# Kernel tuning notes

Hardware: AMD Instinct MI355X
Metric: run time of the kernel (lower is better)

The kernel has to match this reference:

```python
import jax, jax.numpy as jnp
import numpy as np

HEAD_SIZE = 64
NEG_INF = float('-inf')


def setup_inputs() -> dict:
    key = jax.random.key(0)
    ks = jax.random.split(key, 4)
    B, S, H, D = 8, 4096, 1024, HEAD_SIZE
    scale = 1.0 / np.sqrt(H)
    return {
        'x': jax.random.normal(ks[0], (B, S, H), dtype=jnp.float32),
        'Wq': jax.random.normal(ks[1], (H, D), dtype=jnp.float32) * scale,
        'bq': jnp.zeros((D,), dtype=jnp.float32),
        'Wk': jax.random.normal(ks[2], (H, D), dtype=jnp.float32) * scale,
        'bk': jnp.zeros((D,), dtype=jnp.float32),
        'Wv': jax.random.normal(ks[3], (H, D), dtype=jnp.float32) * scale,
        'bv': jnp.zeros((D,), dtype=jnp.float32),
    }


def reference(x, Wq, bq, Wk, bk, Wv, bv):
    # x: [B, S, H]; projections -> [B, S, D]
    B, S, H = x.shape
    q = jnp.einsum('bsh,hd->bsd', x, Wq) + bq
    k = jnp.einsum('bsh,hd->bsd', x, Wk) + bk
    v = jnp.einsum('bsh,hd->bsd', x, Wv) + bv
    # raw scores [B, S, S]
    scores = jnp.einsum('bqd,bkd->bqk', q, k)
    # causal mask applied BEFORE scaling (matches original; -inf/scale == -inf)
    causal = jnp.tril(jnp.ones((S, S), dtype=bool))
    scores = jnp.where(causal, scores, NEG_INF)
    scale = 1.0 / jnp.sqrt(jnp.asarray(q.shape[-1], dtype=scores.dtype))
    attn = jax.nn.softmax(scores * scale, axis=-1)
    # dropout = 0.0 (eval) -> identity
    return jnp.einsum('bqk,bkd->bqd', attn, v)
```

## Files before the change

### kernel.cpp

```cpp
#include <hip/hip_runtime.h>
#include <hip/hip_bf16.h>
#include <math.h>

#define SEQ 4096
#define HID 1024
#define DH  64
#define NB  8
#define QSCALE 0.18033688011112042f

typedef unsigned short ushort_t;
typedef unsigned int   uint_t;
typedef __attribute__((ext_vector_type(8)))  short  bf16x8;
typedef __attribute__((ext_vector_type(4)))  float  f32x4;
typedef __attribute__((ext_vector_type(16))) float  f32x16;
typedef __attribute__((ext_vector_type(4)))  uint_t u32x4;
typedef __attribute__((ext_vector_type(2)))  uint_t u32x2;

static __device__ __forceinline__ ushort_t f2bf(float f) {
    __hip_bfloat16 h = __float2bfloat16(f);
    return *reinterpret_cast<ushort_t*>(&h);
}
static __device__ __forceinline__ ushort_t f2bf_fast(float f) {
    uint_t u = __float_as_uint(f);
    return (ushort_t)((u + 0x8000u) >> 16);
}
static __device__ __forceinline__ uint_t bfpair(float lo, float hi) {
    return (uint_t)f2bf_fast(lo) | ((uint_t)f2bf_fast(hi) << 16);
}

static __device__ __forceinline__ void gld_lds16(const void* g, void* s) {
    __builtin_amdgcn_global_load_lds(
        (const __attribute__((address_space(1))) void*)g,
        (__attribute__((address_space(3))) void*)s, 16, 0, 0);
}

__global__ __launch_bounds__(256) void prep_w(
    const float* __restrict__ Wq, const float* __restrict__ Wk,
    const float* __restrict__ Wv, ushort_t* __restrict__ wts)
{
    __shared__ ushort_t tr[64][72];
    const int bx   = blockIdx.x;
    const int mmat = bx >> 4;
    const int kt   = bx & 15;
    const float* W  = (mmat == 0) ? Wq : (mmat == 1) ? Wk : Wv;
    const float  sc = (mmat == 0) ? QSCALE : 1.0f;

    const int t  = threadIdx.x;
    const int kr = t >> 2, kc = (t & 3) * 16;
    const float* src = W + (size_t)(kt * 64 + kr) * DH + kc;
    float4 a0 = *(const float4*)(src);
    float4 a1 = *(const float4*)(src + 4);
    float4 a2 = *(const float4*)(src + 8);
    float4 a3 = *(const float4*)(src + 12);
    float vv[16] = {a0.x,a0.y,a0.z,a0.w, a1.x,a1.y,a1.z,a1.w,
                    a2.x,a2.y,a2.z,a2.w, a3.x,a3.y,a3.z,a3.w};
    #pragma unroll
    for (int i = 0; i < 16; ++i) tr[kr][kc + i] = f2bf(vv[i] * sc);
    __syncthreads();

    const int cl = t >> 2, jc = (t & 3) * 16;
    const int c  = mmat * 64 + cl;
    ushort_t* dst = wts + kt * 12288 + c * 64;
    #pragma unroll
    for (int jj = 0; jj < 16; ++jj) {
        int j = jc + jj;
        dst[((j >> 3) ^ (cl & 7)) * 8 + (j & 7)] = tr[j][cl];
    }
}

__global__ __launch_bounds__(256) void qkv_proj(
    const float* __restrict__ x, const ushort_t* __restrict__ wts,
    const float* __restrict__ bq, const float* __restrict__ bk,
    const float* __restrict__ bv,
    ushort_t* __restrict__ qimg, ushort_t* __restrict__ kimg,
    ushort_t* __restrict__ vimg)
{
    __shared__ ushort_t bw[2][12288];

    const int t  = threadIdx.x;
    const int w  = t >> 6, l = t & 63, lr = l & 15, g = l >> 4;
    const int row0 = blockIdx.x * 64;
    const int row  = row0 + w * 16 + lr;
    const int ch0 = (g ^ (lr & 7)) * 8;
    const int ch1 = ((g + 4) ^ (lr & 7)) * 8;

    f32x4 acc[12];
    #pragma unroll
    for (int i = 0; i < 12; ++i) acc[i] = (f32x4){0.f,0.f,0.f,0.f};

    const char* wbase = (const char*)wts;
    const int   wlo   = w * 1024 + l * 16;
    const float* xrow = x + (size_t)row * HID + g * 8;

    float4 Xa0, Xa1, Xb0, Xb1;
    {
        Xa0 = *(const float4*)(xrow);
        Xa1 = *(const float4*)(xrow + 4);
        Xb0 = *(const float4*)(xrow + 32);
        Xb1 = *(const float4*)(xrow + 36);
        char* bdst = (char*)&bw[0][0] + w * 1024;
        #pragma unroll
        for (int i = 0; i < 6; ++i)
            gld_lds16(wbase + wlo + i * 4096, bdst + i * 4096);
    }

    for (int kt = 0; kt < 16; ++kt) {
        const int buf = kt & 1;
        __syncthreads();
        float4 Na0, Na1, Nb0, Nb1;
        if (kt < 15) {
            const float* xn = xrow + (kt + 1) * 64;
            Na0 = *(const float4*)(xn);
            Na1 = *(const float4*)(xn + 4);
            Nb0 = *(const float4*)(xn + 32);
            Nb1 = *(const float4*)(xn + 36);
            char* bdst = (char*)&bw[buf ^ 1][0] + w * 1024;
            const char* bsrc = wbase + (size_t)(kt + 1) * 24576 + wlo;
            #pragma unroll
            for (int i = 0; i < 6; ++i)
                gld_lds16(bsrc + i * 4096, bdst + i * 4096);
        }
        bf16x8 af0, af1;
        {
            u32x4 p;
            p.x = bfpair(Xa0.x, Xa0.y); p.y = bfpair(Xa0.z, Xa0.w);
            p.z = bfpair(Xa1.x, Xa1.y); p.w = bfpair(Xa1.z, Xa1.w);
            af0 = *(bf16x8*)&p;
            u32x4 q;
            q.x = bfpair(Xb0.x, Xb0.y); q.y = bfpair(Xb0.z, Xb0.w);
            q.z = bfpair(Xb1.x, Xb1.y); q.w = bfpair(Xb1.z, Xb1.w);
            af1 = *(bf16x8*)&q;
        }
        #pragma unroll
        for (int ct = 0; ct < 12; ++ct) {
            const int c = ct * 16 + lr;
            bf16x8 b0 = *(bf16x8*)&bw[buf][c * 64 + ch0];
            bf16x8 b1 = *(bf16x8*)&bw[buf][c * 64 + ch1];
            acc[ct] = __builtin_amdgcn_mfma_f32_16x16x32_bf16(af0, b0, acc[ct], 0, 0, 0);
            acc[ct] = __builtin_amdgcn_mfma_f32_16x16x32_bf16(af1, b1, acc[ct], 0, 0, 0);
        }
        Xa0 = Na0; Xa1 = Na1; Xb0 = Nb0; Xb1 = Nb1;
    }

    #pragma unroll
    for (int ct = 0; ct < 12; ++ct) {
        const int c    = ct * 16 + lr;
        const int mmat = c >> 6;
        const int cc   = c & 63;
        const float* bp = (mmat == 0) ? bq : (mmat == 1) ? bk : bv;
        const float bias = bp[cc] * (mmat == 0 ? QSCALE : 1.0f);
        #pragma unroll
        for (int r = 0; r < 4; ++r) {
            const int s = row0 + w * 16 + g * 4 + r;
            const ushort_t v = f2bf_fast(acc[ct][r] + bias);
            if (mmat == 0)
                qimg[(size_t)s * 64 + cc] = v;
            else if (mmat == 1)
                kimg[(size_t)(s >> 6) * 4096 + (s & 63) * 64 +
                     ((cc >> 3) ^ (s & 7)) * 8 + (cc & 7)] = v;
            else
                vimg[(size_t)(s >> 6) * 4096 + (size_t)cc * 64 +
                     (((s & 63) >> 3) ^ (cc & 7)) * 8 + (s & 7)] = v;
        }
    }
}

__global__ __launch_bounds__(256) void attn(
    const ushort_t* __restrict__ qimg, const ushort_t* __restrict__ kimg,
    const ushort_t* __restrict__ vimg,
    float* __restrict__ Opart, float* __restrict__ Lpart)
{
    __shared__ ushort_t kvs[2][8192];
    __shared__ float    osc[4096];
    __shared__ float    lred[2][32];

    const int t  = threadIdx.x;
    const int w  = t >> 6, l = t & 63, lw = l & 31, hs = l >> 5;
    const int qh = w & 1;
    const int kh = w >> 1;
    const int bx   = blockIdx.x;
    const int half = bx & 1;
    const int u    = bx >> 1;
    const int qt   = 63 - (u >> 3);
    const int b    = u & 7;
    const int q0   = qt * 64;
    const int n    = qt + 1, hn = n >> 1;
    const int t0   = half ? hn : 0;
    const int t1   = half ? n : hn;
    const int qq   = q0 + qh * 32 + lw;

    bf16x8 qf[4];
    {
        const ushort_t* qp = qimg + (size_t)(b * SEQ + qq) * 64 + hs * 8;
        #pragma unroll
        for (int ks = 0; ks < 4; ++ks) qf[ks] = *(const bf16x8*)(qp + ks * 16);
    }

    f32x16 o0, o1;
    #pragma unroll
    for (int r = 0; r < 16; ++r) { o0[r] = 0.f; o1[r] = 0.f; }
    float lpart = 0.f;

    const char* kbase = (const char*)kimg + (size_t)b * 524288;
    const char* vbase = (const char*)vimg + (size_t)b * 524288;
    const int wo = w * 1024;
    const int lo = l * 16;

    if (t0 < t1) {
        const char* ks = kbase + (size_t)t0 * 8192;
        const char* vs = vbase + (size_t)t0 * 8192;
        char* lk = (char*)&kvs[0][0];
        gld_lds16(ks + wo + lo,        lk + wo);
        gld_lds16(ks + wo + lo + 4096, lk + wo + 4096);
        gld_lds16(vs + wo + lo,        lk + wo + 8192);
        gld_lds16(vs + wo + lo + 4096, lk + wo + 12288);
    }

    for (int kt = t0; kt < t1; ++kt) {
        const int cur = (kt - t0) & 1;
        __syncthreads();
        if (kt + 1 < t1) {
            const char* ks = kbase + (size_t)(kt + 1) * 8192;
            const char* vs = vbase + (size_t)(kt + 1) * 8192;
            char*       lk = (char*)&kvs[cur ^ 1][0];
            gld_lds16(ks + wo + lo,        lk + wo);
            gld_lds16(ks + wo + lo + 4096, lk + wo + 4096);
            gld_lds16(vs + wo + lo,        lk + wo + 8192);
            gld_lds16(vs + wo + lo + 4096, lk + wo + 12288);
        }

        const ushort_t* kb   = &kvs[cur][0];
        const int       krow = kh * 32 + lw;
        const ushort_t* krb  = kb + krow * 64;
        f32x16 s;
        #pragma unroll
        for (int r = 0; r < 16; ++r) s[r] = 0.f;
        #pragma unroll
        for (int ks = 0; ks < 4; ++ks) {
            bf16x8 kf = *(const bf16x8*)(krb + (((ks * 2 + hs) ^ (krow & 7)) * 8));
            s = __builtin_amdgcn_mfma_f32_32x32x16_bf16(kf, qf[ks], s, 0, 0, 0);
        }

        float p[16];
        if (kt == qt) {
            #pragma unroll
            for (int r = 0; r < 16; ++r) {
                const int kvg = kt * 64 + kh * 32 + (r & 3) + 8 * (r >> 2) + 4 * hs;
                p[r] = (kvg > qq) ? 0.f : __builtin_amdgcn_exp2f(s[r]);
            }
        } else {
            #pragma unroll
            for (int r = 0; r < 16; ++r) p[r] = __builtin_amdgcn_exp2f(s[r]);
        }
        {
            float s0 = (p[0] + p[1])  + (p[2] + p[3]);
            float s1 = (p[4] + p[5])  + (p[6] + p[7]);
            float s2 = (p[8] + p[9])  + (p[10] + p[11]);
            float s3 = (p[12] + p[13]) + (p[14] + p[15]);
            lpart += (s0 + s1) + (s2 + s3);
        }

        const ushort_t* vb = &kvs[cur][4096];
        #pragma unroll
        for (int ks2 = 0; ks2 < 2; ++ks2) {
            uint_t a0 = bfpair(p[ks2*8 + 0], p[ks2*8 + 1]);
            uint_t b0 = bfpair(p[ks2*8 + 4], p[ks2*8 + 5]);
            uint_t a1 = bfpair(p[ks2*8 + 2], p[ks2*8 + 3]);
            uint_t b1 = bfpair(p[ks2*8 + 6], p[ks2*8 + 7]);
            asm("v_permlane32_swap_b32 %0, %1" : "+v"(a0), "+v"(b0));
            asm("v_permlane32_swap_b32 %0, %1" : "+v"(a1), "+v"(b1));
            u32x4 pw = { a0, a1, b0, b1 };
            bf16x8 paf = *(bf16x8*)&pw;
            const int sl8 = kh * 4 + ks2 * 2 + hs;
            {
                const int vr0 = lw;
                bf16x8 vf0 = *(const bf16x8*)(vb + vr0 * 64 + ((sl8 ^ (vr0 & 7)) * 8));
                o0 = __builtin_amdgcn_mfma_f32_32x32x16_bf16(paf, vf0, o0, 0, 0, 0);
                const int vr1 = 32 + lw;
                bf16x8 vf1 = *(const bf16x8*)(vb + vr1 * 64 + ((sl8 ^ (vr1 & 7)) * 8));
                o1 = __builtin_amdgcn_mfma_f32_32x32x16_bf16(paf, vf1, o1, 0, 0, 0);
            }
        }
    }

    if (kh == 1) {
        const int lbase = (qh * 64 + l) * 32;
        #pragma unroll
        for (int i = 0; i < 4; ++i) {
            f32x4 v = { o0[4*i], o0[4*i+1], o0[4*i+2], o0[4*i+3] };
            *(f32x4*)&osc[lbase + ((i ^ (l & 7)) * 4)] = v;
        }
        #pragma unroll
        for (int i = 0; i < 4; ++i) {
            f32x4 v = { o1[4*i], o1[4*i+1], o1[4*i+2], o1[4*i+3] };
            *(f32x4*)&osc[lbase + (((i + 4) ^ (l & 7)) * 4)] = v;
        }
        float lsum = lpart + __shfl_xor(lpart, 32);
        if (hs == 0) lred[qh][lw] = lsum;
    }
    __syncthreads();
    if (kh == 0) {
        const int lbase = (qh * 64 + l) * 32;
        #pragma unroll
        for (int i = 0; i < 4; ++i) {
            f32x4 v = *(const f32x4*)&osc[lbase + ((i ^ (l & 7)) * 4)];
            o0[4*i] += v.x; o0[4*i+1] += v.y; o0[4*i+2] += v.z; o0[4*i+3] += v.w;
        }
        #pragma unroll
        for (int i = 0; i < 4; ++i) {
            f32x4 v = *(const f32x4*)&osc[lbase + (((i + 4) ^ (l & 7)) * 4)];
            o1[4*i] += v.x; o1[4*i+1] += v.y; o1[4*i+2] += v.z; o1[4*i+3] += v.w;
        }
        const float lt = (lpart + __shfl_xor(lpart, 32)) + lred[qh][lw];

        const int m = b * 64 + qt;
        float* Op = Opart + ((size_t)half * 512 + m) * 4096;
        #pragma unroll
        for (int r = 0; r < 16; ++r) {
            const int qrow = qh * 32 + (r & 3) + 8 * (r >> 2) + 4 * hs;
            Op[qrow * 64 + lw]      = o0[r];
            Op[qrow * 64 + 32 + lw] = o1[r];
        }
        if (hs == 0)
            Lpart[((size_t)half * 512 + m) * 64 + qh * 32 + lw] = lt;
    }
}

__global__ __launch_bounds__(256) void merge_o(
    const float* __restrict__ Opart, const float* __restrict__ Lpart,
    float* __restrict__ outg)
{
    const int m = blockIdx.x;
    const int b = m >> 6, qt = m & 63;
    const int t = threadIdx.x;
    const int row = t >> 2, c = (t & 3) * 16;

    const float* A = Opart + (size_t)m * 4096 + row * 64 + c;
    const float* B = Opart + (size_t)(512 + m) * 4096 + row * 64 + c;
    const float la = Lpart[(size_t)m * 64 + row];
    const float lb = Lpart[(size_t)(512 + m) * 64 + row];
    const float inv = 1.0f / (la + lb);
    float* dst = outg + ((size_t)b * SEQ + qt * 64 + row) * 64 + c;
    #pragma unroll
    for (int j = 0; j < 4; ++j) {
        float4 va = *(const float4*)(A + j * 4);
        float4 vb = *(const float4*)(B + j * 4);
        float4 vo = { (va.x + vb.x) * inv, (va.y + vb.y) * inv,
                      (va.z + vb.z) * inv, (va.w + vb.w) * inv };
        *(float4*)(dst + j * 4) = vo;
    }
}

extern "C" void kernel_launch(void* const* d_in, const int* in_sizes, int n_in,
                              void* d_out, int out_size, void* d_ws, size_t ws_size,
                              hipStream_t stream) {
    const float* x  = (const float*)d_in[0];
    const float* Wq = (const float*)d_in[1];
    const float* bq = (const float*)d_in[2];
    const float* Wk = (const float*)d_in[3];
    const float* bk = (const float*)d_in[4];
    const float* Wv = (const float*)d_in[5];
    const float* bv = (const float*)d_in[6];
    float* out = (float*)d_out;

    const size_t per = (size_t)NB * SEQ * DH;
    ushort_t* q   = (ushort_t*)d_ws;
    ushort_t* k   = q + per;
    ushort_t* v   = k + per;
    ushort_t* wts = v + per;
    float* Opart  = (float*)((char*)d_ws + (size_t)(16u << 20));
    float* Lpart  = (float*)((char*)d_ws + (size_t)(40u << 20));

    prep_w  <<<dim3(48),   256, 0, stream>>>(Wq, Wk, Wv, wts);
    qkv_proj<<<dim3(512),  256, 0, stream>>>(x, wts, bq, bk, bv, q, k, v);
    attn    <<<dim3(1024), 256, 0, stream>>>(q, k, v, Opart, Lpart);
    merge_o <<<dim3(512),  256, 0, stream>>>(Opart, Lpart, out);
}
```

Before: 257.1 us.

## Use persistent attention blocks with per-batch atomic work queues and XCD affinity

Switches the attention kernel from a fixed 1024-block grid to 768 persistent blocks. Each block pulls work items (query tile and half) from per-batch atomic counters, starting with the batch matching its XCD id so that K/V for one batch stays in that XCD's L2. Items are still issued longest-first. This aims to improve load balance across the triangular causal workload and L2 locality, at the cost of atomic traffic, extra barriers and a counter reset in prep_w.

```diff
diff --git a/kernel.cpp b/kernel.cpp
--- a/kernel.cpp
+++ b/kernel.cpp
@@ -36,8 +36,11 @@
 
 __global__ __launch_bounds__(256) void prep_w(
     const float* __restrict__ Wq, const float* __restrict__ Wk,
-    const float* __restrict__ Wv, ushort_t* __restrict__ wts)
+    const float* __restrict__ Wv, ushort_t* __restrict__ wts,
+    uint_t* __restrict__ cnt)
 {
+    if (blockIdx.x == 0 && threadIdx.x < 8) cnt[threadIdx.x] = 0;
+
     __shared__ ushort_t tr[64][72];
     const int bx   = blockIdx.x;
     const int mmat = bx >> 4;
@@ -168,161 +171,175 @@
 __global__ __launch_bounds__(256) void attn(
     const ushort_t* __restrict__ qimg, const ushort_t* __restrict__ kimg,
     const ushort_t* __restrict__ vimg,
-    float* __restrict__ Opart, float* __restrict__ Lpart)
+    float* __restrict__ Opart, float* __restrict__ Lpart,
+    uint_t* __restrict__ cnt)
 {
     __shared__ ushort_t kvs[2][8192];
     __shared__ float    osc[4096];
     __shared__ float    lred[2][32];
+    __shared__ int      jsh;
 
     const int t  = threadIdx.x;
     const int w  = t >> 6, l = t & 63, lw = l & 31, hs = l >> 5;
     const int qh = w & 1;
     const int kh = w >> 1;
-    const int bx   = blockIdx.x;
-    const int half = bx & 1;
-    const int u    = bx >> 1;
-    const int qt   = 63 - (u >> 3);
-    const int b    = u & 7;
-    const int q0   = qt * 64;
-    const int n    = qt + 1, hn = n >> 1;
-    const int t0   = half ? hn : 0;
-    const int t1   = half ? n : hn;
-    const int qq   = q0 + qh * 32 + lw;
-
-    bf16x8 qf[4];
-    {
-        const ushort_t* qp = qimg + (size_t)(b * SEQ + qq) * 64 + hs * 8;
-        #pragma unroll
-        for (int ks = 0; ks < 4; ++ks) qf[ks] = *(const bf16x8*)(qp + ks * 16);
-    }
-
-    f32x16 o0, o1;
-    #pragma unroll
-    for (int r = 0; r < 16; ++r) { o0[r] = 0.f; o1[r] = 0.f; }
-    float lpart = 0.f;
-
-    const char* kbase = (const char*)kimg + (size_t)b * 524288;
-    const char* vbase = (const char*)vimg + (size_t)b * 524288;
     const int wo = w * 1024;
     const int lo = l * 16;
 
-    if (t0 < t1) {
-        const char* ks = kbase + (size_t)t0 * 8192;
-        const char* vs = vbase + (size_t)t0 * 8192;
-        char* lk = (char*)&kvs[0][0];
-        gld_lds16(ks + wo + lo,        lk + wo);
-        gld_lds16(ks + wo + lo + 4096, lk + wo + 4096);
-        gld_lds16(vs + wo + lo,        lk + wo + 8192);
-        gld_lds16(vs + wo + lo + 4096, lk + wo + 12288);
-    }
-
-    for (int kt = t0; kt < t1; ++kt) {
-        const int cur = (kt - t0) & 1;
-        __syncthreads();
-        if (kt + 1 < t1) {
-            const char* ks = kbase + (size_t)(kt + 1) * 8192;
-            const char* vs = vbase + (size_t)(kt + 1) * 8192;
-            char*       lk = (char*)&kvs[cur ^ 1][0];
-            gld_lds16(ks + wo + lo,        lk + wo);
-            gld_lds16(ks + wo + lo + 4096, lk + wo + 4096);
-            gld_lds16(vs + wo + lo,        lk + wo + 8192);
-            gld_lds16(vs + wo + lo + 4096, lk + wo + 12288);
-        }
-
-        const ushort_t* kb   = &kvs[cur][0];
-        const int       krow = kh * 32 + lw;
-        const ushort_t* krb  = kb + krow * 64;
-        f32x16 s;
-        #pragma unroll
-        for (int r = 0; r < 16; ++r) s[r] = 0.f;
-        #pragma unroll
-        for (int ks = 0; ks < 4; ++ks) {
-            bf16x8 kf = *(const bf16x8*)(krb + (((ks * 2 + hs) ^ (krow & 7)) * 8));
-            s = __builtin_amdgcn_mfma_f32_32x32x16_bf16(kf, qf[ks], s, 0, 0, 0);
-        }
-
-        float p[16];
-        if (kt == qt) {
+    int xcd;
+    { int v; asm("s_getreg_b32 %0, hwreg(HW_REG_XCC_ID)" : "=s"(v)); xcd = v & 7; }
+
+    for (int pass = 0; pass < 8; ++pass) {
+        const int b = (xcd + pass) & 7;
+        const char* kbase = (const char*)kimg + (size_t)b * 524288;
+        const char* vbase = (const char*)vimg + (size_t)b * 524288;
+
+        while (true) {
+            __syncthreads();
+            if (t == 0) jsh = (int)atomicAdd(&cnt[b], 1u);
+            __syncthreads();
+            const int j = jsh;
+            if (j >= 128) break;
+
+            const int qt   = 63 - (j >> 1);
+            const int half = j & 1;
+            const int q0   = qt * 64;
+            const int n    = qt + 1, hn = n >> 1;
+            const int t0   = half ? hn : 0;
+            const int t1   = half ? n : hn;
+            const int qq   = q0 + qh * 32 + lw;
+
+            bf16x8 qf[4];
+            {
+                const ushort_t* qp = qimg + (size_t)(b * SEQ + qq) * 64 + hs * 8;
+                #pragma unroll
+                for (int ks = 0; ks < 4; ++ks) qf[ks] = *(const bf16x8*)(qp + ks * 16);
+            }
+
+            f32x16 o0, o1;
             #pragma unroll
-            for (int r = 0; r < 16; ++r) {
-                const int kvg = kt * 64 + kh * 32 + (r & 3) + 8 * (r >> 2) + 4 * hs;
-                p[r] = (kvg > qq) ? 0.f : __builtin_amdgcn_exp2f(s[r]);
-            }
-        } else {
-            #pragma unroll
-            for (int r = 0; r < 16; ++r) p[r] = __builtin_amdgcn_exp2f(s[r]);
-        }
-        {
-            float s0 = (p[0] + p[1])  + (p[2] + p[3]);
-            float s1 = (p[4] + p[5])  + (p[6] + p[7]);
-            float s2 = (p[8] + p[9])  + (p[10] + p[11]);
-            float s3 = (p[12] + p[13]) + (p[14] + p[15]);
-            lpart += (s0 + s1) + (s2 + s3);
-        }
-
-        const ushort_t* vb = &kvs[cur][4096];
-        #pragma unroll
-        for (int ks2 = 0; ks2 < 2; ++ks2) {
-            uint_t a0 = bfpair(p[ks2*8 + 0], p[ks2*8 + 1]);
-            uint_t b0 = bfpair(p[ks2*8 + 4], p[ks2*8 + 5]);
-            uint_t a1 = bfpair(p[ks2*8 + 2], p[ks2*8 + 3]);
-            uint_t b1 = bfpair(p[ks2*8 + 6], p[ks2*8 + 7]);
-            asm("v_permlane32_swap_b32 %0, %1" : "+v"(a0), "+v"(b0));
-            asm("v_permlane32_swap_b32 %0, %1" : "+v"(a1), "+v"(b1));
-            u32x4 pw = { a0, a1, b0, b1 };
-            bf16x8 paf = *(bf16x8*)&pw;
-            const int sl8 = kh * 4 + ks2 * 2 + hs;
-            {
-                const int vr0 = lw;
-                bf16x8 vf0 = *(const bf16x8*)(vb + vr0 * 64 + ((sl8 ^ (vr0 & 7)) * 8));
-                o0 = __builtin_amdgcn_mfma_f32_32x32x16_bf16(paf, vf0, o0, 0, 0, 0);
-                const int vr1 = 32 + lw;
-                bf16x8 vf1 = *(const bf16x8*)(vb + vr1 * 64 + ((sl8 ^ (vr1 & 7)) * 8));
-                o1 = __builtin_amdgcn_mfma_f32_32x32x16_bf16(paf, vf1, o1, 0, 0, 0);
-            }
-        }
-    }
-
-    if (kh == 1) {
-        const int lbase = (qh * 64 + l) * 32;
-        #pragma unroll
-        for (int i = 0; i < 4; ++i) {
-            f32x4 v = { o0[4*i], o0[4*i+1], o0[4*i+2], o0[4*i+3] };
-            *(f32x4*)&osc[lbase + ((i ^ (l & 7)) * 4)] = v;
-        }
-        #pragma unroll
-        for (int i = 0; i < 4; ++i) {
-            f32x4 v = { o1[4*i], o1[4*i+1], o1[4*i+2], o1[4*i+3] };
-            *(f32x4*)&osc[lbase + (((i + 4) ^ (l & 7)) * 4)] = v;
-        }
-        float lsum = lpart + __shfl_xor(lpart, 32);
-        if (hs == 0) lred[qh][lw] = lsum;
-    }
-    __syncthreads();
-    if (kh == 0) {
-        const int lbase = (qh * 64 + l) * 32;
-        #pragma unroll
-        for (int i = 0; i < 4; ++i) {
-            f32x4 v = *(const f32x4*)&osc[lbase + ((i ^ (l & 7)) * 4)];
-            o0[4*i] += v.x; o0[4*i+1] += v.y; o0[4*i+2] += v.z; o0[4*i+3] += v.w;
-        }
-        #pragma unroll
-        for (int i = 0; i < 4; ++i) {
-            f32x4 v = *(const f32x4*)&osc[lbase + (((i + 4) ^ (l & 7)) * 4)];
-            o1[4*i] += v.x; o1[4*i+1] += v.y; o1[4*i+2] += v.z; o1[4*i+3] += v.w;
-        }
-        const float lt = (lpart + __shfl_xor(lpart, 32)) + lred[qh][lw];
-
-        const int m = b * 64 + qt;
-        float* Op = Opart + ((size_t)half * 512 + m) * 4096;
-        #pragma unroll
-        for (int r = 0; r < 16; ++r) {
-            const int qrow = qh * 32 + (r & 3) + 8 * (r >> 2) + 4 * hs;
-            Op[qrow * 64 + lw]      = o0[r];
-            Op[qrow * 64 + 32 + lw] = o1[r];
-        }
-        if (hs == 0)
-            Lpart[((size_t)half * 512 + m) * 64 + qh * 32 + lw] = lt;
+            for (int r = 0; r < 16; ++r) { o0[r] = 0.f; o1[r] = 0.f; }
+            float lpart = 0.f;
+
+            if (t0 < t1) {
+                const char* ks = kbase + (size_t)t0 * 8192;
+                const char* vs = vbase + (size_t)t0 * 8192;
+                char* lk = (char*)&kvs[0][0];
+                gld_lds16(ks + wo + lo,        lk + wo);
+                gld_lds16(ks + wo + lo + 4096, lk + wo + 4096);
+                gld_lds16(vs + wo + lo,        lk + wo + 8192);
+                gld_lds16(vs + wo + lo + 4096, lk + wo + 12288);
+            }
+
+            for (int kt = t0; kt < t1; ++kt) {
+                const int cur = (kt - t0) & 1;
+                __syncthreads();
+                if (kt + 1 < t1) {
+                    const char* ks = kbase + (size_t)(kt + 1) * 8192;
+                    const char* vs = vbase + (size_t)(kt + 1) * 8192;
+                    char*       lk = (char*)&kvs[cur ^ 1][0];
+                    gld_lds16(ks + wo + lo,        lk + wo);
+                    gld_lds16(ks + wo + lo + 4096, lk + wo + 4096);
+                    gld_lds16(vs + wo + lo,        lk + wo + 8192);
+                    gld_lds16(vs + wo + lo + 4096, lk + wo + 12288);
+                }
+
+                const ushort_t* kb   = &kvs[cur][0];
+                const int       krow = kh * 32 + lw;
+                const ushort_t* krb  = kb + krow * 64;
+                f32x16 s;
+                #pragma unroll
+                for (int r = 0; r < 16; ++r) s[r] = 0.f;
+                #pragma unroll
+                for (int ks = 0; ks < 4; ++ks) {
+                    bf16x8 kf = *(const bf16x8*)(krb + (((ks * 2 + hs) ^ (krow & 7)) * 8));
+                    s = __builtin_amdgcn_mfma_f32_32x32x16_bf16(kf, qf[ks], s, 0, 0, 0);
+                }
+
+                float p[16];
+                if (kt == qt) {
+                    #pragma unroll
+                    for (int r = 0; r < 16; ++r) {
+                        const int kvg = kt * 64 + kh * 32 + (r & 3) + 8 * (r >> 2) + 4 * hs;
+                        p[r] = (kvg > qq) ? 0.f : __builtin_amdgcn_exp2f(s[r]);
+                    }
+                } else {
+                    #pragma unroll
+                    for (int r = 0; r < 16; ++r) p[r] = __builtin_amdgcn_exp2f(s[r]);
+                }
+                {
+                    float s0 = (p[0] + p[1])  + (p[2] + p[3]);
+                    float s1 = (p[4] + p[5])  + (p[6] + p[7]);
+                    float s2 = (p[8] + p[9])  + (p[10] + p[11]);
+                    float s3 = (p[12] + p[13]) + (p[14] + p[15]);
+                    lpart += (s0 + s1) + (s2 + s3);
+                }
+
+                const ushort_t* vb = &kvs[cur][4096];
+                #pragma unroll
+                for (int ks2 = 0; ks2 < 2; ++ks2) {
+                    uint_t a0 = bfpair(p[ks2*8 + 0], p[ks2*8 + 1]);
+                    uint_t b0 = bfpair(p[ks2*8 + 4], p[ks2*8 + 5]);
+                    uint_t a1 = bfpair(p[ks2*8 + 2], p[ks2*8 + 3]);
+                    uint_t b1 = bfpair(p[ks2*8 + 6], p[ks2*8 + 7]);
+                    asm("v_permlane32_swap_b32 %0, %1" : "+v"(a0), "+v"(b0));
+                    asm("v_permlane32_swap_b32 %0, %1" : "+v"(a1), "+v"(b1));
+                    u32x4 pw = { a0, a1, b0, b1 };
+                    bf16x8 paf = *(bf16x8*)&pw;
+                    const int sl8 = kh * 4 + ks2 * 2 + hs;
+                    {
+                        const int vr0 = lw;
+                        bf16x8 vf0 = *(const bf16x8*)(vb + vr0 * 64 + ((sl8 ^ (vr0 & 7)) * 8));
+                        o0 = __builtin_amdgcn_mfma_f32_32x32x16_bf16(paf, vf0, o0, 0, 0, 0);
+                        const int vr1 = 32 + lw;
+                        bf16x8 vf1 = *(const bf16x8*)(vb + vr1 * 64 + ((sl8 ^ (vr1 & 7)) * 8));
+                        o1 = __builtin_amdgcn_mfma_f32_32x32x16_bf16(paf, vf1, o1, 0, 0, 0);
+                    }
+                }
+            }
+
+            if (kh == 1) {
+                const int lbase = (qh * 64 + l) * 32;
+                #pragma unroll
+                for (int i = 0; i < 4; ++i) {
+                    f32x4 v = { o0[4*i], o0[4*i+1], o0[4*i+2], o0[4*i+3] };
+                    *(f32x4*)&osc[lbase + ((i ^ (l & 7)) * 4)] = v;
+                }
+                #pragma unroll
+                for (int i = 0; i < 4; ++i) {
+                    f32x4 v = { o1[4*i], o1[4*i+1], o1[4*i+2], o1[4*i+3] };
+                    *(f32x4*)&osc[lbase + (((i + 4) ^ (l & 7)) * 4)] = v;
+                }
+                float lsum = lpart + __shfl_xor(lpart, 32);
+                if (hs == 0) lred[qh][lw] = lsum;
+            }
+            __syncthreads();
+            if (kh == 0) {
+                const int lbase = (qh * 64 + l) * 32;
+                #pragma unroll
+                for (int i = 0; i < 4; ++i) {
+                    f32x4 v = *(const f32x4*)&osc[lbase + ((i ^ (l & 7)) * 4)];
+                    o0[4*i] += v.x; o0[4*i+1] += v.y; o0[4*i+2] += v.z; o0[4*i+3] += v.w;
+                }
+                #pragma unroll
+                for (int i = 0; i < 4; ++i) {
+                    f32x4 v = *(const f32x4*)&osc[lbase + (((i + 4) ^ (l & 7)) * 4)];
+                    o1[4*i] += v.x; o1[4*i+1] += v.y; o1[4*i+2] += v.z; o1[4*i+3] += v.w;
+                }
+                const float lt = (lpart + __shfl_xor(lpart, 32)) + lred[qh][lw];
+
+                const int m = b * 64 + qt;
+                float* Op = Opart + ((size_t)half * 512 + m) * 4096;
+                #pragma unroll
+                for (int r = 0; r < 16; ++r) {
+                    const int qrow = qh * 32 + (r & 3) + 8 * (r >> 2) + 4 * hs;
+                    Op[qrow * 64 + lw]      = o0[r];
+                    Op[qrow * 64 + 32 + lw] = o1[r];
+                }
+                if (hs == 0)
+                    Lpart[((size_t)half * 512 + m) * 64 + qh * 32 + lw] = lt;
+            }
+        }
     }
 }
 
@@ -370,9 +387,10 @@
     ushort_t* wts = v + per;
     float* Opart  = (float*)((char*)d_ws + (size_t)(16u << 20));
     float* Lpart  = (float*)((char*)d_ws + (size_t)(40u << 20));
-
-    prep_w  <<<dim3(48),   256, 0, stream>>>(Wq, Wk, Wv, wts);
-    qkv_proj<<<dim3(512),  256, 0, stream>>>(x, wts, bq, bk, bv, q, k, v);
-    attn    <<<dim3(1024), 256, 0, stream>>>(q, k, v, Opart, Lpart);
-    merge_o <<<dim3(512),  256, 0, stream>>>(Opart, Lpart, out);
-}
+    uint_t* cnt   = (uint_t*)((char*)d_ws + (size_t)(41u << 20));
+
+    prep_w  <<<dim3(48),  256, 0, stream>>>(Wq, Wk, Wv, wts, cnt);
+    qkv_proj<<<dim3(512), 256, 0, stream>>>(x, wts, bq, bk, bv, q, k, v);
+    attn    <<<dim3(768), 256, 0, stream>>>(q, k, v, Opart, Lpart, cnt);
+    merge_o <<<dim3(512), 256, 0, stream>>>(Opart, Lpart, out);
+}
```

After: 330.1 us. 28.4% more time.

## Deepen attention KV prefetch to three stages with explicit vmcnt waits

Applied to the files above, without the earlier changes.

The attention kernel moves from a double-buffered to a triple-buffered K/V LDS pipeline. It prefetches two tiles ahead and uses partial s_waitcnt vmcnt counts with raw s_barrier instead of __syncthreads, so a full drain happens only on the last tiles. The output/row-sum reduction scratch now aliases the KV buffers to keep LDS usage bounded. The projection kernel also issues weight loads before x loads and uses partial vmcnt waits plus barriers, so the next tile's loads stay in flight during the MFMAs. The risk is in the hand-counted vmcnt values, which must match the number of outstanding loads, and in the extra LDS, which could lower occupancy.

```diff
diff --git a/kernel.cpp b/kernel.cpp
--- a/kernel.cpp
+++ b/kernel.cpp
@@ -106,20 +106,24 @@
 
     for (int kt = 0; kt < 16; ++kt) {
         const int buf = kt & 1;
-        __syncthreads();
         float4 Na0, Na1, Nb0, Nb1;
         if (kt < 15) {
+            char* bdst = (char*)&bw[buf ^ 1][0] + w * 1024;
+            const char* bsrc = wbase + (size_t)(kt + 1) * 24576 + wlo;
+            #pragma unroll
+            for (int i = 0; i < 6; ++i)
+                gld_lds16(bsrc + i * 4096, bdst + i * 4096);
             const float* xn = xrow + (kt + 1) * 64;
             Na0 = *(const float4*)(xn);
             Na1 = *(const float4*)(xn + 4);
             Nb0 = *(const float4*)(xn + 32);
             Nb1 = *(const float4*)(xn + 36);
-            char* bdst = (char*)&bw[buf ^ 1][0] + w * 1024;
-            const char* bsrc = wbase + (size_t)(kt + 1) * 24576 + wlo;
-            #pragma unroll
-            for (int i = 0; i < 6; ++i)
-                gld_lds16(bsrc + i * 4096, bdst + i * 4096);
-        }
+        }
+        if (kt < 15) asm volatile("s_waitcnt vmcnt(10)" ::: "memory");
+        else         asm volatile("s_waitcnt vmcnt(0)"  ::: "memory");
+        __builtin_amdgcn_s_barrier();
+        asm volatile("" ::: "memory");
+
         bf16x8 af0, af1;
         {
             u32x4 p;
@@ -139,6 +143,8 @@
             acc[ct] = __builtin_amdgcn_mfma_f32_16x16x32_bf16(af0, b0, acc[ct], 0, 0, 0);
             acc[ct] = __builtin_amdgcn_mfma_f32_16x16x32_bf16(af1, b1, acc[ct], 0, 0, 0);
         }
+        asm volatile("" ::: "memory");
+        __builtin_amdgcn_s_barrier();
         Xa0 = Na0; Xa1 = Na1; Xb0 = Nb0; Xb1 = Nb1;
     }
 
@@ -170,9 +176,9 @@
     const ushort_t* __restrict__ vimg,
     float* __restrict__ Opart, float* __restrict__ Lpart)
 {
-    __shared__ ushort_t kvs[2][8192];
-    __shared__ float    osc[4096];
-    __shared__ float    lred[2][32];
+    __shared__ ushort_t kvs[3][8192];
+    float* const oscp  = (float*)&kvs[0][0];
+    float* const lredp = (float*)&kvs[1][0];
 
     const int t  = threadIdx.x;
     const int w  = t >> 6, l = t & 63, lw = l & 31, hs = l >> 5;
@@ -206,28 +212,28 @@
     const int wo = w * 1024;
     const int lo = l * 16;
 
-    if (t0 < t1) {
-        const char* ks = kbase + (size_t)t0 * 8192;
-        const char* vs = vbase + (size_t)t0 * 8192;
-        char* lk = (char*)&kvs[0][0];
+    auto STAGE = [&](int ss, int tt) {
+        const char* ks = kbase + (size_t)tt * 8192;
+        const char* vs = vbase + (size_t)tt * 8192;
+        char* lk = (char*)&kvs[ss][0];
         gld_lds16(ks + wo + lo,        lk + wo);
         gld_lds16(ks + wo + lo + 4096, lk + wo + 4096);
         gld_lds16(vs + wo + lo,        lk + wo + 8192);
         gld_lds16(vs + wo + lo + 4096, lk + wo + 12288);
-    }
-
+    };
+
+    if (t0     < t1) STAGE(0, t0);
+    if (t0 + 1 < t1) STAGE(1, t0 + 1);
+
+    int cur = 0;
     for (int kt = t0; kt < t1; ++kt) {
-        const int cur = (kt - t0) & 1;
-        __syncthreads();
-        if (kt + 1 < t1) {
-            const char* ks = kbase + (size_t)(kt + 1) * 8192;
-            const char* vs = vbase + (size_t)(kt + 1) * 8192;
-            char*       lk = (char*)&kvs[cur ^ 1][0];
-            gld_lds16(ks + wo + lo,        lk + wo);
-            gld_lds16(ks + wo + lo + 4096, lk + wo + 4096);
-            gld_lds16(vs + wo + lo,        lk + wo + 8192);
-            gld_lds16(vs + wo + lo + 4096, lk + wo + 12288);
-        }
+        const int sd = (cur == 0) ? 2 : cur - 1;
+        if (kt + 2 < t1) STAGE(sd, kt + 2);
+        if      (kt + 2 < t1) asm volatile("s_waitcnt vmcnt(8)" ::: "memory");
+        else if (kt + 1 < t1) asm volatile("s_waitcnt vmcnt(4)" ::: "memory");
+        else                  asm volatile("s_waitcnt vmcnt(0)" ::: "memory");
+        __builtin_amdgcn_s_barrier();
+        asm volatile("" ::: "memory");
 
         const ushort_t* kb   = &kvs[cur][0];
         const int       krow = kh * 32 + lw;
@@ -281,6 +287,9 @@
                 o1 = __builtin_amdgcn_mfma_f32_32x32x16_bf16(paf, vf1, o1, 0, 0, 0);
             }
         }
+        asm volatile("" ::: "memory");
+        __builtin_amdgcn_s_barrier();
+        cur = (cur == 2) ? 0 : cur + 1;
     }
 
     if (kh == 1) {
@@ -288,30 +297,30 @@
         #pragma unroll
         for (int i = 0; i < 4; ++i) {
             f32x4 v = { o0[4*i], o0[4*i+1], o0[4*i+2], o0[4*i+3] };
-            *(f32x4*)&osc[lbase + ((i ^ (l & 7)) * 4)] = v;
+            *(f32x4*)&oscp[lbase + ((i ^ (l & 7)) * 4)] = v;
         }
         #pragma unroll
         for (int i = 0; i < 4; ++i) {
             f32x4 v = { o1[4*i], o1[4*i+1], o1[4*i+2], o1[4*i+3] };
-            *(f32x4*)&osc[lbase + (((i + 4) ^ (l & 7)) * 4)] = v;
+            *(f32x4*)&oscp[lbase + (((i + 4) ^ (l & 7)) * 4)] = v;
         }
         float lsum = lpart + __shfl_xor(lpart, 32);
-        if (hs == 0) lred[qh][lw] = lsum;
+        if (hs == 0) lredp[qh * 32 + lw] = lsum;
     }
     __syncthreads();
     if (kh == 0) {
         const int lbase = (qh * 64 + l) * 32;
         #pragma unroll
         for (int i = 0; i < 4; ++i) {
-            f32x4 v = *(const f32x4*)&osc[lbase + ((i ^ (l & 7)) * 4)];
+            f32x4 v = *(const f32x4*)&oscp[lbase + ((i ^ (l & 7)) * 4)];
             o0[4*i] += v.x; o0[4*i+1] += v.y; o0[4*i+2] += v.z; o0[4*i+3] += v.w;
         }
         #pragma unroll
         for (int i = 0; i < 4; ++i) {
-            f32x4 v = *(const f32x4*)&osc[lbase + (((i + 4) ^ (l & 7)) * 4)];
+            f32x4 v = *(const f32x4*)&oscp[lbase + (((i + 4) ^ (l & 7)) * 4)];
             o1[4*i] += v.x; o1[4*i+1] += v.y; o1[4*i+2] += v.z; o1[4*i+3] += v.w;
         }
-        const float lt = (lpart + __shfl_xor(lpart, 32)) + lred[qh][lw];
+        const float lt = (lpart + __shfl_xor(lpart, 32)) + lredp[qh * 32 + lw];
 
         const int m = b * 64 + qt;
         float* Op = Opart + ((size_t)half * 512 + m) * 4096;
```

Measured after the change: 252.0 us. 2.0% less time.
